# Optimization experiments

Hardware: AMD Instinct MI355X
Metric: run time of the kernel (lower is better)

The kernel has to match this reference:

```python
import jax, jax.numpy as jnp
import numpy as np
from jax.scipy.special import gammaln

# NQ_IN + 4 == 2*H is required because the two kernel=1, padding=1 convs grow the
# length axis by 4 and the following nn.Linear(2H, H) acts on the length axis.
B, NQ_IN, NK, QDIM, KDIM, H = 16, 2044, 1024, 80, 256, 1024


def setup_inputs() -> dict:
    ks = jax.random.split(jax.random.key(0), 14)
    s = 0.02
    return {
        "query": jax.random.normal(ks[0], (B, NQ_IN, QDIM), jnp.float32),
        "key": jax.random.normal(ks[1], (B, NK, KDIM), jnp.float32),
        "query_lens": jnp.full((B,), 2 * H, jnp.int32),
        "key_lens": jnp.full((B,), NK, jnp.int32),
        # query branch params (Conv1d k=1 stored as (out,in); Linear as (out,in))
        "qc1_w": jax.random.normal(ks[2], (2 * H, QDIM), jnp.float32) * s,
        "qc1_b": jax.random.normal(ks[3], (2 * H,), jnp.float32) * s,
        "qc2_w": jax.random.normal(ks[4], (2 * H, 2 * H), jnp.float32) * s,
        "qc2_b": jax.random.normal(ks[5], (2 * H,), jnp.float32) * s,
        "ql_w": jax.random.normal(ks[6], (H, 2 * H), jnp.float32) * s,
        "ql_b": jax.random.normal(ks[7], (H,), jnp.float32) * s,
        # key branch params
        "kc_w": jax.random.normal(ks[8], (H, KDIM, 3), jnp.float32) * s,
        "kc_b": jax.random.normal(ks[9], (H,), jnp.float32) * s,
        "kl1_w": jax.random.normal(ks[10], (2 * H, H), jnp.float32) * s,
        "kl1_b": jax.random.normal(ks[11], (2 * H,), jnp.float32) * s,
        "kl2_w": jax.random.normal(ks[12], (H, 2 * H), jnp.float32) * s,
        "kl2_b": jax.random.normal(ks[13], (H,), jnp.float32) * s,
    }


def _log_beta_binom(query_lens, key_lens, tq, tk):
    # Standard MAS beta-binomial alignment prior over a (tq, tk) grid.
    i = jnp.arange(tq, dtype=jnp.float32)[None, :, None]
    j = jnp.arange(tk, dtype=jnp.float32)[None, None, :]
    ql = query_lens.astype(jnp.float32)[:, None, None]
    kl = key_lens.astype(jnp.float32)[:, None, None]
    a = i + 1.0
    b = jnp.maximum(ql - i, 1.0)
    n = jnp.maximum(kl - 1.0, 0.0)
    nmj = jnp.maximum(n - j, 0.0)

    def betaln(x, y):
        return gammaln(x) + gammaln(y) - gammaln(x + y)

    logp = (gammaln(n + 1.0) - gammaln(j + 1.0) - gammaln(nmj + 1.0)
            + betaln(j + a, nmj + b) - betaln(a, b))
    valid = (i < ql) & (j < kl)
    return jnp.where(valid, logp, -1e9)


def _forward(query, key, query_lens, key_lens,
             qc1_w, qc1_b, qc2_w, qc2_b, ql_w, ql_b,
             kc_w, kc_b, kl1_w, kl1_b, kl2_w, kl2_b):
    # query branch: b n c -> b c n, two k=1/p=1 convs (pad length, pointwise), Linear over LENGTH axis
    q = jnp.transpose(query, (0, 2, 1))                       # (B, QDIM, NQ_IN)
    q = jnp.pad(q, ((0, 0), (0, 0), (1, 1)))
    q = jnp.einsum('bcn,oc->bon', q, qc1_w) + qc1_b[None, :, None]   # (B, 2H, NQ_IN+2)
    q = jnp.pad(q, ((0, 0), (0, 0), (1, 1)))
    q = jnp.einsum('bcn,oc->bon', q, qc2_w) + qc2_b[None, :, None]   # (B, 2H, 2H)
    q = jnp.einsum('bcn,hn->bch', q, ql_w) + ql_b                    # (B, 2H, H) Linear on length axis

    # key branch: b n c -> b c n, Conv1d k=3 p=1, then two Linears over LENGTH axis
    k = jnp.transpose(key, (0, 2, 1))                         # (B, KDIM, NK)
    k = jax.lax.conv_general_dilated(k, kc_w, (1,), ((1, 1),),
                                     dimension_numbers=('NCH', 'OIH', 'NCH'))
    k = k + kc_b[None, :, None]                               # (B, H, NK=H)
    k = jnp.einsum('bcn,on->bco', k, kl1_w) + kl1_b           # (B, H, 2H)
    k = jnp.einsum('bco,ho->bch', k, kl2_w) + kl2_b           # (B, H, H)

    # dist = -cdist(q, k), computed via the GEMM form (same as torch.cdist mm mode)
    sq = (jnp.sum(q * q, -1)[:, :, None] + jnp.sum(k * k, -1)[:, None, :]
          - 2.0 * jnp.einsum('bnd,bmd->bnm', q, k))           # (B, 2H, H)
    dist = -jnp.sqrt(jnp.maximum(sq, 1e-12))

    prior = _log_beta_binom(query_lens, key_lens, q.shape[1], k.shape[1])
    return jax.nn.log_softmax(dist + prior, axis=-1)


def reference(query, key, query_lens, key_lens,
              qc1_w, qc1_b, qc2_w, qc2_b, ql_w, ql_b,
              kc_w, kc_b, kl1_w, kl1_b, kl2_w, kl2_b):
    return _forward(query, key, query_lens, key_lens,
                    qc1_w, qc1_b, qc2_w, qc2_b, ql_w, ql_b,
                    kc_w, kc_b, kl1_w, kl1_b, kl2_w, kl2_b)
```

## Files before the change

### kernel.cpp

```cpp
#include <hip/hip_runtime.h>
#include <math.h>

typedef unsigned short u16;
typedef float floatx4 __attribute__((ext_vector_type(4)));
typedef __bf16 bf16x8 __attribute__((ext_vector_type(8)));

#define BB   16
#define TQ   2048
#define TK   1024
#define HH   1024
#define H2   2048
#define QD   80
#define QDP  128
#define KD   256
#define NQ   2044
#define NKEY 1024
#define T12N 3072

__device__ __forceinline__ u16 f2bf(float f) {
  unsigned int u = __float_as_uint(f);
  u = u + 0x7fffu + ((u >> 16) & 1u);
  return (u16)(u >> 16);
}
__device__ __forceinline__ float bf2f(u16 s) {
  return __uint_as_float(((unsigned int)s) << 16);
}
__device__ __forceinline__ float tgf(const float* __restrict__ tbl, int x) {
  return tbl[(x < 8191) ? (x < 0 ? 0 : x) : 8191];
}

__global__ __launch_bounds__(256) void prep_all_k(
    const float* __restrict__ qc2_w, const float* __restrict__ kl2_w,
    const float* __restrict__ ql_w, const float* __restrict__ kc_w,
    const float* __restrict__ kl1_w,
    u16* __restrict__ qc2w, u16* __restrict__ kl2w, u16* __restrict__ qlw2,
    u16* __restrict__ kcp, float* __restrict__ colsum1, float* __restrict__ tbl)
{
  long b = blockIdx.x;
  const int t = threadIdx.x;
  __shared__ float red[256];
  if (b < 16384) {
    long i = b * 256 + t; qc2w[i] = f2bf(qc2_w[i]); return;
  }
  b -= 16384;
  if (b < 8192) {
    long i = b * 256 + t; kl2w[i] = f2bf(kl2_w[i]); return;
  }
  b -= 8192;
  if (b < 8192) {
    long i = b * 256 + t;
    int n = (int)(i & 2047);
    int h = (int)(i >> 11);
    qlw2[i] = (n < NQ) ? f2bf(ql_w[(long)h * H2 + n + 2]) : (u16)0; return;
  }
  b -= 8192;
  if (b < 3072) {
    long i = b * 256 + t;
    int r = (int)(i % 768);
    int o = (int)(i / 768);
    int tt = r >> 8, d = r & 255;
    kcp[i] = f2bf(kc_w[((long)o * KD + d) * 3 + tt]); return;
  }
  b -= 3072;
  if (b < 2048) {
    const float* row = kl1_w + b * (long)HH;
    float s = row[t] + row[t + 256] + row[t + 512] + row[t + 768];
    red[t] = s; __syncthreads();
    for (int st = 128; st > 0; st >>= 1) { if (t < st) red[t] += red[t + st]; __syncthreads(); }
    if (!t) colsum1[b] = red[0];
    return;
  }
  b -= 2048;
  { int i = (int)(b * 256 + t); if (i < 8192) tbl[i] = i ? (float)lgamma((double)i) : 0.0f; }
}

__global__ __launch_bounds__(256) void tpack_k(
    const float* __restrict__ kl1_w, const float* __restrict__ qc1_w,
    const float* __restrict__ query,
    u16* __restrict__ kl1T, u16* __restrict__ qc1T, u16* __restrict__ qT)
{
  __shared__ float tile[64][65];
  int bid = blockIdx.x;
  const int tid = threadIdx.x;
  const int r4 = tid >> 6, c = tid & 63;
  const float* src; u16* dst;
  int sr0, sc0, srcR, srcC, srcStride, dstC;
  if (bid < 512) {
    sr0 = (bid >> 4) * 64; sc0 = (bid & 15) * 64;
    src = kl1_w; srcR = 2048; srcC = 1024; srcStride = 1024;
    dst = kl1T; dstC = 2048;
  } else if ((bid -= 512) < 64) {
    sr0 = (bid >> 1) * 64; sc0 = (bid & 1) * 64;
    src = qc1_w; srcR = 2048; srcC = QD; srcStride = QD;
    dst = qc1T; dstC = 2048;
  } else {
    bid -= 64;
    const int b16 = bid >> 6, r = bid & 63;
    sr0 = (r >> 1) * 64; sc0 = (r & 1) * 64;
    src = query + (long)b16 * NQ * QD; srcR = NQ; srcC = QD; srcStride = QD;
    dst = qT + (long)b16 * QDP * 2048; dstC = 2048;
  }
#pragma unroll
  for (int rr = r4; rr < 64; rr += 4) {
    const int gr = sr0 + rr, gc = sc0 + c;
    tile[rr][c] = (gr < srcR && gc < srcC) ? src[(long)gr * srcStride + gc] : 0.f;
  }
  __syncthreads();
#pragma unroll
  for (int rr = r4; rr < 64; rr += 4)
    dst[(long)(sc0 + rr) * dstC + sr0 + c] = f2bf(tile[c][rr]);
}

__global__ __launch_bounds__(256) void pack_kcolT_k(const float* __restrict__ key, u16* __restrict__ out) {
  __shared__ float tile[64][65];
  const int bid = blockIdx.x, tid = threadIdx.x;
  const int b = bid >> 6, r = bid & 63;
  const int m0 = (r >> 2) * 64;
  const int d0 = (r & 3) * 64;
  const int r4 = tid >> 6, c = tid & 63;
#pragma unroll
  for (int rr = r4; rr < 64; rr += 4)
    tile[rr][c] = key[((long)b * NKEY + m0 + rr) * KD + d0 + c];
  __syncthreads();
#pragma unroll
  for (int t = 0; t < 3; t++) {
    const int n = m0 + 1 - t + c;
    if (n >= 0 && n < NKEY) {
#pragma unroll
      for (int rr = r4; rr < 64; rr += 4)
        out[((long)b * 768 + t * 256 + d0 + rr) * NKEY + n] = f2bf(tile[c][rr]);
    }
  }
  if (m0 == 0 && c == 0) {
#pragma unroll
    for (int rr = r4; rr < 64; rr += 4)
      out[((long)b * 768 + d0 + rr) * NKEY + 0] = (u16)0;
  }
  if (m0 == 960 && c == 0) {
#pragma unroll
    for (int rr = r4; rr < 64; rr += 4)
      out[((long)b * 768 + 512 + d0 + rr) * NKEY + (NKEY - 1)] = (u16)0;
  }
}

__global__ __launch_bounds__(256) void fold_bias_k(
    const float* __restrict__ qc2_w, const float* __restrict__ qc1_b, const float* __restrict__ qc2_b,
    const float* __restrict__ kl2_w, const float* __restrict__ kl1_b, const float* __restrict__ kl2_b,
    const float* __restrict__ ql_w, const float* __restrict__ colsum1,
    float* __restrict__ bqm, float* __restrict__ bkv, float* __restrict__ s1v, float* __restrict__ s0v,
    float* __restrict__ wsum)
{
  const int bid = blockIdx.x, t = threadIdx.x;
  float s = 0.f, s2 = 0.f;
  if (bid < H2) {
    const float* row = qc2_w + (long)bid * H2;
    for (int k = t; k < H2; k += 256) s += row[k] * qc1_b[k];
  } else if (bid < H2 + HH) {
    const float* row = kl2_w + (long)(bid - H2) * H2;
    for (int k = t; k < H2; k += 256) { const float rv = row[k]; s += rv * kl1_b[k]; s2 += rv * colsum1[k]; }
  } else {
    const float* row = ql_w + (long)(bid - H2 - HH) * H2;
    for (int m = 1 + t; m <= H2 - 2; m += 256) s += row[m];
  }
  __shared__ float red[256];
  __shared__ float red2[256];
  red[t] = s; red2[t] = s2; __syncthreads();
  for (int st = 128; st > 0; st >>= 1) {
    if (t < st) { red[t] += red[t + st]; red2[t] += red2[t + st]; }
    __syncthreads();
  }
  if (!t) {
    if (bid < H2) bqm[bid] = red[0] + qc2_b[bid];
    else if (bid < H2 + HH) { bkv[bid - H2] = red[0] + kl2_b[bid - H2]; wsum[bid - H2] = red2[0]; }
    else {
      int h = bid - H2 - HH;
      s1v[h] = red[0];
      s0v[h] = ql_w[(long)h * H2] + ql_w[(long)h * H2 + H2 - 1];
    }
  }
}

__device__ __forceinline__ void gld_lds16(const u16* g, u16* l) {
  __builtin_amdgcn_global_load_lds((const __attribute__((address_space(1))) void*)g,
                                   (__attribute__((address_space(3))) void*)l, 16, 0, 0);
}

template<int OUTF32>
__global__ __launch_bounds__(256) void gemm_bt(
    const u16* __restrict__ A, const u16* __restrict__ B, void* __restrict__ Cv,
    int M, int N, int K, int lda, int ldb, int swap, int kspl,
    long sA, long sB, long sC, long sN,
    const float* __restrict__ colb, const float* __restrict__ rowb,
    const float* __restrict__ r1m, const float* __restrict__ r1n,
    const float* __restrict__ r2m, const float* __restrict__ r2n)
{
  __shared__ __align__(16) u16 As[128 * 32];
  __shared__ __align__(16) u16 Bs[128 * 32];
  const int bz = blockIdx.z;
  const int bb_ = (kspl > 1) ? bz / kspl : bz;
  const int ks_ = (kspl > 1) ? bz - bb_ * kspl : 0;
  const int tid  = threadIdx.x;
  const int lane = tid & 63;
  const int wv = tid >> 6;
  const int wm = ((tid >> 7) & 1) * 64;
  const int wn = ((tid >> 6) & 1) * 64;
  const int m0 = (swap ? blockIdx.x : blockIdx.y) * 128;
  const int n0 = (swap ? blockIdx.y : blockIdx.x) * 128;

  const int srow = wv * 32 + (lane >> 2);
  const int scol = (lane & 3) << 3;
  const u16* ga = A + bb_ * sA + (long)ks_ * K + (long)(m0 + srow) * lda + scol;
  const u16* gb = B + bb_ * sB + (long)ks_ * K + (long)(n0 + srow) * ldb + scol;
  u16* la0 = &As[(wv * 32) * 32];
  u16* la1 = &As[(wv * 32 + 16) * 32];
  u16* lb0 = &Bs[(wv * 32) * 32];
  u16* lb1 = &Bs[(wv * 32 + 16) * 32];
  const long a16 = (long)16 * lda;
  const long b16 = (long)16 * ldb;

  floatx4 acc[4][4];
#pragma unroll
  for (int a_ = 0; a_ < 4; a_++)
#pragma unroll
    for (int b_ = 0; b_ < 4; b_++) acc[a_][b_] = (floatx4){0.f, 0.f, 0.f, 0.f};

  const int fr = lane & 15;
  const int fk = (lane >> 4) << 3;

  for (int kb = 0; kb < K; kb += 32) {
    gld_lds16(ga,       la0);
    gld_lds16(ga + a16, la1);
    gld_lds16(gb,       lb0);
    gld_lds16(gb + b16, lb1);
    ga += 32; gb += 32;
    __syncthreads();
    bf16x8 af[4], bfr[4];
#pragma unroll
    for (int mi = 0; mi < 4; mi++)
      af[mi] = *reinterpret_cast<const bf16x8*>(&As[(wm + mi * 16 + fr) * 32 + fk]);
#pragma unroll
    for (int ni = 0; ni < 4; ni++)
      bfr[ni] = *reinterpret_cast<const bf16x8*>(&Bs[(wn + ni * 16 + fr) * 32 + fk]);
#pragma unroll
    for (int mi = 0; mi < 4; mi++)
#pragma unroll
      for (int ni = 0; ni < 4; ni++)
        acc[mi][ni] = __builtin_amdgcn_mfma_f32_16x16x32_bf16(af[mi], bfr[ni], acc[mi][ni], 0, 0, 0);
    __syncthreads();
  }

  const int fr4 = (lane >> 4) << 2;
  const int fc  = lane & 15;
  u16*   Cb16 = (u16*)Cv + (long)bz * sC;
  float* Cb32 = (float*)Cv + (long)bz * sC;
  const float* cbp  = colb ? colb + (long)bb_ * sN : nullptr;
  const float* r1np = r1n ? r1n + (long)bb_ * sN : nullptr;
  const float* r2np = r2n ? r2n + (long)bb_ * sN : nullptr;
#pragma unroll
  for (int mi = 0; mi < 4; mi++) {
#pragma unroll
    for (int ni = 0; ni < 4; ni++) {
      const int gm0 = m0 + wm + mi * 16 + fr4;
      const int gn  = n0 + wn + ni * 16 + fc;
      const float cbv  = cbp ? cbp[gn] : 0.f;
      const float r1nv = r1np ? r1np[gn] : 0.f;
      const float r2nv = r2np ? r2np[gn] : 0.f;
#pragma unroll
      for (int rr = 0; rr < 4; rr++) {
        const int gm = gm0 + rr;
        float v = acc[mi][ni][rr] + cbv;
        if (rowb) v += rowb[gm];
        if (r1m)  v += r1m[gm] * r1nv;
        if (r2m)  v += r2m[gm] * r2nv;
        if (OUTF32) Cb32[(long)gm * N + gn] = v;
        else        Cb16[(long)gm * N + gn] = f2bf(v);
      }
    }
  }
}

__global__ __launch_bounds__(256) void reduce_bk_k(const float* __restrict__ P, u16* __restrict__ out,
                                                   long chunk, int S, long total) {
  long j = ((long)blockIdx.x * 256 + threadIdx.x) * 4;
  if (j >= total) return;
  long b = j / chunk;
  const float* p = P + j + b * chunk * (S - 1);
  float4 s = *reinterpret_cast<const float4*>(p);
  for (int t = 1; t < S; t++) {
    const float4 v = *reinterpret_cast<const float4*>(p + (long)t * chunk);
    s.x += v.x; s.y += v.y; s.z += v.z; s.w += v.w;
  }
  union { u16 h[4]; uint2 u; } o;
  o.h[0] = f2bf(s.x); o.h[1] = f2bf(s.y); o.h[2] = f2bf(s.z); o.h[3] = f2bf(s.w);
  *reinterpret_cast<uint2*>(out + j) = o.u;
}

__global__ __launch_bounds__(256) void u_k(
    const u16* __restrict__ TpT, const float* __restrict__ qlb,
    const float* __restrict__ s1, const float* __restrict__ s0,
    const float* __restrict__ tbl, const int* __restrict__ qlens, const int* __restrict__ klens,
    float* __restrict__ u0, float* __restrict__ u1, float* __restrict__ u2,
    float* __restrict__ sc, float* __restrict__ c1,
    float* __restrict__ crow, float* __restrict__ t12)
{
  const int bid = blockIdx.x, t = threadIdx.x;
  __shared__ float4 red[256];
  if (bid < BB * QDP) {
    uint2 v = reinterpret_cast<const uint2*>(TpT + (long)bid * HH)[t];
    float a0 = bf2f((u16)(v.x & 0xffff)), a1 = bf2f((u16)(v.x >> 16));
    float a2 = bf2f((u16)(v.y & 0xffff)), a3 = bf2f((u16)(v.y >> 16));
    float4 q  = reinterpret_cast<const float4*>(qlb)[t];
    float4 w1 = reinterpret_cast<const float4*>(s1)[t];
    float4 w0 = reinterpret_cast<const float4*>(s0)[t];
    float4 s;
    s.x = a0 * q.x  + a1 * q.y  + a2 * q.z  + a3 * q.w;
    s.y = a0 * w1.x + a1 * w1.y + a2 * w1.z + a3 * w1.w;
    s.z = a0 * w0.x + a1 * w0.y + a2 * w0.z + a3 * w0.w;
    s.w = 0.f;
    red[t] = s; __syncthreads();
    for (int st = 128; st > 0; st >>= 1) {
      if (t < st) { red[t].x += red[t + st].x; red[t].y += red[t + st].y; red[t].z += red[t + st].z; }
      __syncthreads();
    }
    if (!t) { u0[bid] = red[0].x; u1[bid] = red[0].y; u2[bid] = red[0].z; }
  } else if (bid < BB * QDP + 6) {
    const int idx = bid - BB * QDP;
    const float* X = (idx == 1 || idx == 5) ? s1 : (idx == 2) ? s0 : qlb;
    const float* Y = (idx == 1 || idx == 3) ? s1 : (idx == 0) ? qlb : s0;
    float4 x = reinterpret_cast<const float4*>(X)[t];
    float4 y = reinterpret_cast<const float4*>(Y)[t];
    float4 s; s.x = x.x * y.x + x.y * y.y + x.z * y.z + x.w * y.w; s.y = s.z = s.w = 0.f;
    red[t] = s; __syncthreads();
    for (int st = 128; st > 0; st >>= 1) {
      if (t < st) red[t].x += red[t + st].x;
      __syncthreads();
    }
    if (!t) sc[idx] = red[0].x;
  } else if (bid < BB * QDP + 6 + 64) {
    const int idx = bid - (BB * QDP + 6);
    const int b = idx >> 2;
    const int j = ((idx & 3) << 8) | t;
    const int kl = klens[b];
    const int n_ = (kl - 1 > 0) ? kl - 1 : 0;
    c1[b * TK + j] = tgf(tbl, j + 1) + tgf(tbl, n_ - j + 1);
  } else if (bid < BB * QDP + 6 + 64 + 128) {
    const int idx = bid - (BB * QDP + 6 + 64);
    const int b = idx >> 3;
    const int i = ((idx & 7) << 8) | t;
    const int ql = qlens[b], kl = klens[b];
    const int n_ = (kl - 1 > 0) ? kl - 1 : 0;
    const int bb = (ql - i > 1) ? ql - i : 1;
    crow[b * TQ + i] = tgf(tbl, n_ + 1) + tgf(tbl, i + 1 + bb) - tgf(tbl, i + 1)
                     - tgf(tbl, bb) - tgf(tbl, i + 1 + n_ + bb);
  } else {
    const int idx = bid - (BB * QDP + 6 + 64 + 128);
    const int b = idx / 12;
    const int s = (idx - b * 12) * 256 + t;
    const int ql = qlens[b], kl = klens[b];
    const int n_ = (kl - 1 > 0) ? kl - 1 : 0;
    t12[b * T12N + s] = tgf(tbl, s + 1) + tgf(tbl, n_ + ql - s);
  }
}

__global__ __launch_bounds__(256) void qn_k(
    const u16* __restrict__ Wq, const float* __restrict__ WqG,
    const float* __restrict__ u0, const float* __restrict__ u1, const float* __restrict__ u2,
    const float* __restrict__ bqm, const float* __restrict__ qc2_b,
    const float* __restrict__ sc, float* __restrict__ qn)
{
  const int bx = blockIdx.x, t = threadIdx.x;
  const int b = bx >> 10;
  const int i = ((bx & 1023) << 1) | (t >> 7);
  const int d = t & 127;
  const float w  = bf2f(Wq[(long)i * QDP + d]);
  const float g  = WqG[((long)b * H2 + i) * QDP + d];
  const float bq = bqm[i], q2 = qc2_b[i];
  const float uu = u0[b * QDP + d] + bq * u1[b * QDP + d] + q2 * u2[b * QDP + d];
  __shared__ float red[256];
  red[t] = w * (g + 2.f * uu); __syncthreads();
  for (int s = 64; s > 0; s >>= 1) { if ((t & 127) < s) red[t] += red[t + s]; __syncthreads(); }
  if (d == 0) {
    const float cst = sc[0] + bq * bq * sc[1] + q2 * q2 * sc[2]
                    + 2.f * (bq * sc[3] + q2 * sc[4] + bq * q2 * sc[5]);
    qn[b * TQ + i] = red[t] + cst;
  }
}

__global__ __launch_bounds__(256) void rownormk_k(
    const u16* __restrict__ K3, const float* __restrict__ qlb,
    const float* __restrict__ s1, const float* __restrict__ s0,
    float* __restrict__ kn, float* __restrict__ yb, float* __restrict__ y1, float* __restrict__ y0)
{
  const long r = blockIdx.x;
  const int t = threadIdx.x;
  uint2 v = reinterpret_cast<const uint2*>(K3 + r * HH)[t];
  float a0 = bf2f((u16)(v.x & 0xffff)), a1 = bf2f((u16)(v.x >> 16));
  float a2 = bf2f((u16)(v.y & 0xffff)), a3 = bf2f((u16)(v.y >> 16));
  float4 q  = reinterpret_cast<const float4*>(qlb)[t];
  float4 w1 = reinterpret_cast<const float4*>(s1)[t];
  float4 w0 = reinterpret_cast<const float4*>(s0)[t];
  float4 s;
  s.x = a0 * a0   + a1 * a1   + a2 * a2   + a3 * a3;
  s.y = a0 * q.x  + a1 * q.y  + a2 * q.z  + a3 * q.w;
  s.z = a0 * w1.x + a1 * w1.y + a2 * w1.z + a3 * w1.w;
  s.w = a0 * w0.x + a1 * w0.y + a2 * w0.z + a3 * w0.w;
  __shared__ float4 red[256];
  red[t] = s; __syncthreads();
  for (int st = 128; st > 0; st >>= 1) {
    if (t < st) {
      red[t].x += red[t + st].x; red[t].y += red[t + st].y;
      red[t].z += red[t + st].z; red[t].w += red[t + st].w;
    }
    __syncthreads();
  }
  if (!t) { kn[r] = red[0].x; yb[r] = red[0].y; y1[r] = red[0].z; y0[r] = red[0].w; }
}

#define L2E 1.4426950408889634f
__global__ __launch_bounds__(512) void smax_k(
    const u16* __restrict__ Wq, const u16* __restrict__ Z2, float* __restrict__ out,
    const float* __restrict__ ybv, const float* __restrict__ y1v, const float* __restrict__ y0v,
    const float* __restrict__ bqmv, const float* __restrict__ qc2_b,
    const float* __restrict__ qnv, const float* __restrict__ knv, const float* __restrict__ c1v,
    const float* __restrict__ crowv, const float* __restrict__ t12v,
    const int* __restrict__ qlens, const int* __restrict__ klens)
{
  __shared__ float vst[64][132];
  __shared__ float t12s[1088];
  __shared__ float qns[64], crs[64], bqms[64], q2bs[64];
  __shared__ float2 lseb[4][64];
  __shared__ float lsef[64];

  const int mt = blockIdx.x, b = blockIdx.y;
  const int m0 = mt * 64;
  const int t = threadIdx.x;
  const int w = t >> 6, lane = t & 63;
  const int wm2 = (w >> 2) * 32;
  const int wn2 = (w & 3) * 32;
  const int fr = lane & 15, fk = (lane >> 4) << 3;
  const int fr4 = (lane >> 4) << 2, fc = lane & 15;
  const int qlv = qlens[b], klv = klens[b];

  if (t < 64) {
    qns[t]  = qnv[(long)b * TQ + m0 + t];
    crs[t]  = crowv[(long)b * TQ + m0 + t];
    bqms[t] = bqmv[m0 + t];
    q2bs[t] = qc2_b[m0 + t];
  }
  for (int k = t; k < 1088; k += 512) t12s[k] = t12v[(long)b * T12N + m0 + k];

  bf16x8 af[4][2];
#pragma unroll
  for (int kc = 0; kc < 4; kc++)
#pragma unroll
    for (int mi = 0; mi < 2; mi++)
      af[kc][mi] = *reinterpret_cast<const bf16x8*>(
          Wq + (long)(m0 + wm2 + mi * 16 + fr) * QDP + kc * 32 + fk);

  const u16* Zb = Z2 + (long)b * TK * QDP;
  const float* ybp = ybv + (long)b * TK;
  const float* y1p = y1v + (long)b * TK;
  const float* y0p = y0v + (long)b * TK;
  const float* knp = knv + (long)b * TK;
  const float* c1p = c1v + (long)b * TK;
  float* outp = out + (long)b * TQ * TK + (long)m0 * TK;

  float m_[8], s_[8];
#pragma unroll
  for (int ri = 0; ri < 8; ri++) { m_[ri] = -3.0e38f; s_[ri] = 0.f; }

  __syncthreads();

  for (int pass = 0; pass < 2; pass++) {
    for (int nt = 0; nt < 8; nt++) {
      bf16x8 bfr[4][2];
#pragma unroll
      for (int kc = 0; kc < 4; kc++)
#pragma unroll
        for (int nj = 0; nj < 2; nj++)
          bfr[kc][nj] = *reinterpret_cast<const bf16x8*>(
              Zb + (long)(nt * 128 + wn2 + nj * 16 + fr) * QDP + kc * 32 + fk);

      floatx4 acc[2][2];
#pragma unroll
      for (int mi = 0; mi < 2; mi++)
#pragma unroll
        for (int nj = 0; nj < 2; nj++) acc[mi][nj] = (floatx4){0.f, 0.f, 0.f, 0.f};
#pragma unroll
      for (int kc = 0; kc < 4; kc++)
#pragma unroll
        for (int mi = 0; mi < 2; mi++)
#pragma unroll
          for (int nj = 0; nj < 2; nj++)
            acc[mi][nj] = __builtin_amdgcn_mfma_f32_16x16x32_bf16(af[kc][mi], bfr[kc][nj], acc[mi][nj], 0, 0, 0);

      int gj[2]; float ybj[2], y1j[2], y0j[2], knj[2], c1j[2];
#pragma unroll
      for (int nj = 0; nj < 2; nj++) {
        gj[nj]  = nt * 128 + wn2 + nj * 16 + fc;
        ybj[nj] = ybp[gj[nj]]; y1j[nj] = y1p[gj[nj]]; y0j[nj] = y0p[gj[nj]];
        knj[nj] = knp[gj[nj]]; c1j[nj] = c1p[gj[nj]];
      }

#pragma unroll
      for (int mi = 0; mi < 2; mi++) {
#pragma unroll
        for (int rr = 0; rr < 4; rr++) {
          const int rl = wm2 + mi * 16 + fr4 + rr;
          const float qnr = qns[rl], crr = crs[rl], bqr = bqms[rl], q2r = q2bs[rl];
          float vv[2];
#pragma unroll
          for (int nj = 0; nj < 2; nj++) {
            const float Sv = acc[mi][nj][rr] + ybj[nj] + bqr * y1j[nj] + q2r * y0j[nj];
            const float sq = fmaxf(qnr + knj[nj] - 2.0f * Sv, 1e-12f);
            const float x = -__builtin_amdgcn_sqrtf(sq) + crr - c1j[nj] + t12s[rl + gj[nj]];
            vv[nj] = ((m0 + rl) < qlv && gj[nj] < klv) ? x : -1e9f;
          }
          const int ri = mi * 4 + rr;
          if (pass == 0) {
            const float nm = fmaxf(m_[ri], fmaxf(vv[0], vv[1]));
            s_[ri] = s_[ri] * exp2f((m_[ri] - nm) * L2E)
                   + exp2f((vv[0] - nm) * L2E) + exp2f((vv[1] - nm) * L2E);
            m_[ri] = nm;
          } else {
            const float l = lsef[rl];
            acc[mi][0][rr] = vv[0] - l;
            acc[mi][1][rr] = vv[1] - l;
          }
        }
      }

      if (pass == 1) {
#pragma unroll
        for (int mi = 0; mi < 2; mi++)
#pragma unroll
          for (int nj = 0; nj < 2; nj++)
#pragma unroll
            for (int rr = 0; rr < 4; rr++)
              vst[wm2 + mi * 16 + fr4 + rr][wn2 + nj * 16 + fc] = acc[mi][nj][rr];
        __syncthreads();
#pragma unroll
        for (int k = 0; k < 4; k++) {
          const int fi = k * 512 + t;
          const int row = fi >> 5, lc4 = (fi & 31) << 2;
          *reinterpret_cast<float4*>(outp + (long)row * TK + nt * 128 + lc4) =
              *reinterpret_cast<const float4*>(&vst[row][lc4]);
        }
        __syncthreads();
      }
    }

    if (pass == 0) {
#pragma unroll
      for (int k2 = 1; k2 <= 8; k2 <<= 1) {
#pragma unroll
        for (int ri = 0; ri < 8; ri++) {
          const float om = __shfl_xor(m_[ri], k2, 64);
          const float os = __shfl_xor(s_[ri], k2, 64);
          const float nm = fmaxf(m_[ri], om);
          s_[ri] = s_[ri] * exp2f((m_[ri] - nm) * L2E) + os * exp2f((om - nm) * L2E);
          m_[ri] = nm;
        }
      }
      if (fc == 0) {
#pragma unroll
        for (int mi = 0; mi < 2; mi++)
#pragma unroll
          for (int rr = 0; rr < 4; rr++)
            lseb[w & 3][wm2 + mi * 16 + fr4 + rr] = make_float2(m_[mi * 4 + rr], s_[mi * 4 + rr]);
      }
      __syncthreads();
      if (t < 64) {
        const float2 e0 = lseb[0][t], e1 = lseb[1][t], e2 = lseb[2][t], e3 = lseb[3][t];
        const float mm = fmaxf(fmaxf(e0.x, e1.x), fmaxf(e2.x, e3.x));
        const float ss = e0.y * exp2f((e0.x - mm) * L2E) + e1.y * exp2f((e1.x - mm) * L2E)
                       + e2.y * exp2f((e2.x - mm) * L2E) + e3.y * exp2f((e3.x - mm) * L2E);
        lsef[t] = mm + logf(ss);
      }
      __syncthreads();
    }
  }
}

extern "C" void kernel_launch(void* const* d_in, const int* in_sizes, int n_in,
                              void* d_out, int out_size, void* d_ws, size_t ws_size,
                              hipStream_t stream)
{
  (void)in_sizes; (void)n_in; (void)out_size; (void)ws_size;
  const float* query = (const float*)d_in[0];
  const float* key   = (const float*)d_in[1];
  const int*   qlens = (const int*)d_in[2];
  const int*   klens = (const int*)d_in[3];
  const float* qc1_w = (const float*)d_in[4];
  const float* qc1_b = (const float*)d_in[5];
  const float* qc2_w = (const float*)d_in[6];
  const float* qc2_b = (const float*)d_in[7];
  const float* ql_w  = (const float*)d_in[8];
  const float* ql_b  = (const float*)d_in[9];
  const float* kc_w  = (const float*)d_in[10];
  const float* kc_b  = (const float*)d_in[11];
  const float* kl1_w = (const float*)d_in[12];
  const float* kl1_b = (const float*)d_in[13];
  const float* kl2_w = (const float*)d_in[14];
  const float* kl2_b = (const float*)d_in[15];

  size_t off = 0;
  char* ws = (char*)d_ws;
  auto alloc = [&](size_t bytes) -> char* {
    char* p = ws + off; off += (bytes + 255) & ~(size_t)255; return p;
  };
  u16* qc2w_bf = (u16*)alloc(2ull * H2 * H2);
  u16* qc1T_bf = (u16*)alloc(2ull * QDP * H2);
  u16* kl2w_bf = (u16*)alloc(2ull * HH * H2);
  u16* kl1T_bf = (u16*)alloc(2ull * HH * H2);
  u16* qT_bf   = (u16*)alloc(2ull * BB * QDP * 2048);
  u16* kcolT_bf= (u16*)d_ws;
  u16* Z2_bf   = (u16*)d_ws;
  u16* qlw2_bf = (u16*)alloc(2ull * HH * 2048);
  u16* kcp_bf  = (u16*)alloc(2ull * HH * 768);
  u16* TpT_bf  = (u16*)alloc(2ull * H2 * HH);
  char* pool   = alloc(2ull * BB * HH * NKEY);
  float* Pbuf  = (float*)pool;
  u16* X_bf    = (u16*)pool;
  float* tbl  = (float*)alloc(4ull * 8192);
  u16* Wq_bf  = (u16*)alloc(2ull * H2 * QDP);
  u16* Wk_bf  = (u16*)alloc(2ull * HH * NKEY);
  float* bqm  = (float*)alloc(4ull * H2);
  float* bkv  = (float*)alloc(4ull * HH);
  float* s1v  = (float*)alloc(4ull * HH);
  float* s0v  = (float*)alloc(4ull * HH);
  float* wsum = (float*)alloc(4ull * HH);
  float* colsum1 = (float*)alloc(4ull * H2);
  u16* K3_bf  = (u16*)alloc(2ull * BB * TK * HH);
  float* qnv  = (float*)alloc(4ull * BB * TQ);
  float* knv  = (float*)alloc(4ull * BB * TK);
  float* ybv  = (float*)alloc(4ull * BB * TK);
  float* y1v  = (float*)alloc(4ull * BB * TK);
  float* y0v  = (float*)alloc(4ull * BB * TK);
  float* u0v  = (float*)alloc(4ull * BB * QDP);
  float* u1v  = (float*)alloc(4ull * BB * QDP);
  float* u2v  = (float*)alloc(4ull * BB * QDP);
  float* c1v  = (float*)alloc(4ull * BB * TK);
  float* crowv= (float*)alloc(4ull * BB * TQ);
  float* t12v = (float*)alloc(4ull * BB * T12N);
  float* scv  = (float*)alloc(256);
  float* WqG  = (float*)d_out;
  u16* G_bf   = (u16*)((char*)d_out + 16777216);

  prep_all_k<<<37920, 256, 0, stream>>>(qc2_w, kl2_w, ql_w, kc_w, kl1_w,
                                        qc2w_bf, kl2w_bf, qlw2_bf, kcp_bf, colsum1, tbl);
  tpack_k<<<1600, 256, 0, stream>>>(kl1_w, qc1_w, query, kl1T_bf, qc1T_bf, qT_bf);
  fold_bias_k<<<4096, 256, 0, stream>>>(qc2_w, qc1_b, qc2_b, kl2_w, kl1_b, kl2_b, ql_w, colsum1,
                                        bqm, bkv, s1v, s0v, wsum);

  gemm_bt<1><<<dim3(1, 16, 16), 256, 0, stream>>>(qc2w_bf, qc1T_bf, Pbuf, H2, QDP, 128,
      H2, H2, 0, 16, 0, 0, (long)H2 * QDP, 0,
      nullptr, nullptr, nullptr, nullptr, nullptr, nullptr);
  reduce_bk_k<<<256, 256, 0, stream>>>(Pbuf, Wq_bf, (long)H2 * QDP, 16, (long)H2 * QDP);

  gemm_bt<1><<<dim3(8, 8, 8), 256, 0, stream>>>(kl2w_bf, kl1T_bf, Pbuf, HH, NKEY, 256,
      H2, H2, 0, 8, 0, 0, (long)HH * NKEY, 0,
      nullptr, nullptr, nullptr, nullptr, nullptr, nullptr);
  reduce_bk_k<<<1024, 256, 0, stream>>>(Pbuf, Wk_bf, (long)HH * NKEY, 8, (long)HH * NKEY);

  gemm_bt<1><<<dim3(8, 16, 4), 256, 0, stream>>>(qT_bf, qlw2_bf, Pbuf, H2, HH, 512,
      2048, 2048, 0, 4, 0, 0, (long)H2 * HH, 0,
      nullptr, nullptr, nullptr, nullptr, nullptr, nullptr);
  reduce_bk_k<<<2048, 256, 0, stream>>>(Pbuf, TpT_bf, (long)H2 * HH, 4, (long)H2 * HH);

  gemm_bt<1><<<dim3(1, 1, 128), 256, 0, stream>>>(TpT_bf, TpT_bf, Pbuf, 128, 128, 128,
      HH, HH, 0, 8, (long)QDP * HH, (long)QDP * HH, 128 * 128, 0,
      nullptr, nullptr, nullptr, nullptr, nullptr, nullptr);
  reduce_bk_k<<<256, 256, 0, stream>>>(Pbuf, G_bf, 128 * 128, 8, (long)BB * 128 * 128);

  gemm_bt<1><<<dim3(1, 16, 16), 256, 0, stream>>>(Wq_bf, G_bf, WqG, H2, QDP, QDP,
      QDP, QDP, 0, 1, 0, (long)QDP * QDP, (long)H2 * QDP, 0,
      nullptr, nullptr, nullptr, nullptr, nullptr, nullptr);
  u_k<<<BB * QDP + 6 + 64 + 128 + 192, 256, 0, stream>>>(TpT_bf, ql_b, s1v, s0v, tbl, qlens, klens,
                                                         u0v, u1v, u2v, scv, c1v, crowv, t12v);
  qn_k<<<BB * TQ / 2, 256, 0, stream>>>(Wq_bf, WqG, u0v, u1v, u2v, bqm, qc2_b, scv, qnv);

  pack_kcolT_k<<<1024, 256, 0, stream>>>(key, kcolT_bf);
  gemm_bt<0><<<dim3(6, 8, BB), 256, 0, stream>>>(Wk_bf, kcolT_bf, X_bf, HH, 768, NKEY,
      NKEY, NKEY, 0, 1, 0, (long)768 * NKEY, (long)HH * 768, 0,
      nullptr, nullptr, nullptr, nullptr, nullptr, nullptr);
  gemm_bt<0><<<dim3(8, 8, BB), 256, 0, stream>>>(kcp_bf, X_bf, K3_bf, HH, NKEY, 768,
      768, 768, 1, 1, 0, (long)HH * 768, (long)TK * HH, 0,
      bkv, nullptr, kc_b, wsum, nullptr, nullptr);

  gemm_bt<1><<<dim3(8, 1, 32), 256, 0, stream>>>(K3_bf, TpT_bf, Pbuf, TK, QDP, 512,
      HH, HH, 1, 2, (long)TK * HH, (long)QDP * HH, (long)TK * QDP, 0,
      nullptr, nullptr, nullptr, nullptr, nullptr, nullptr);
  reduce_bk_k<<<2048, 256, 0, stream>>>(Pbuf, Z2_bf, (long)TK * QDP, 2, (long)BB * TK * QDP);

  rownormk_k<<<BB * TK, 256, 0, stream>>>(K3_bf, ql_b, s1v, s0v, knv, ybv, y1v, y0v);

  smax_k<<<dim3(32, 16), 512, 0, stream>>>(Wq_bf, Z2_bf, (float*)d_out,
      ybv, y1v, y0v, bqm, qc2_b, qnv, knv, c1v, crowv, t12v, qlens, klens);
}
```

Baseline: 634.4 us.

## Enlarge softmax tile to 128 rows, stage column terms in LDS, store directly

The fused distance/log-softmax kernel now runs 1024 threads per block, each block covering 128 query rows instead of 64, so the grid halves to 256 blocks. Per-column terms (key norm, bias projections, c1) are folded and preloaded into shared memory once per block, replacing repeated global loads in both passes. The LDS-staged float4 output write with its two barriers per tile is replaced by direct scalar stores from the MFMA accumulator layout. Risks: only 256 blocks for the whole GPU, and the scalar stores are less coalesced than the previous float4 stores.

```diff
diff --git a/kernel.cpp b/kernel.cpp
--- a/kernel.cpp
+++ b/kernel.cpp
@@ -417,7 +417,7 @@
 }
 
 #define L2E 1.4426950408889634f
-__global__ __launch_bounds__(512) void smax_k(
+__global__ __launch_bounds__(1024) void smax_k(
     const u16* __restrict__ Wq, const u16* __restrict__ Z2, float* __restrict__ out,
     const float* __restrict__ ybv, const float* __restrict__ y1v, const float* __restrict__ y0v,
     const float* __restrict__ bqmv, const float* __restrict__ qc2_b,
@@ -425,14 +425,14 @@
     const float* __restrict__ crowv, const float* __restrict__ t12v,
     const int* __restrict__ qlens, const int* __restrict__ klens)
 {
-  __shared__ float vst[64][132];
-  __shared__ float t12s[1088];
-  __shared__ float qns[64], crs[64], bqms[64], q2bs[64];
-  __shared__ float2 lseb[4][64];
-  __shared__ float lsef[64];
+  __shared__ float t12s[1152];
+  __shared__ float jA[1024], jB[1024], jC[1024], jc1[1024];
+  __shared__ float qns[128], crs[128], bqms[128], q2bs[128];
+  __shared__ float2 lseb[4][128];
+  __shared__ float lsef[128];
 
   const int mt = blockIdx.x, b = blockIdx.y;
-  const int m0 = mt * 64;
+  const int m0 = mt * 128;
   const int t = threadIdx.x;
   const int w = t >> 6, lane = t & 63;
   const int wm2 = (w >> 2) * 32;
@@ -441,13 +441,24 @@
   const int fr4 = (lane >> 4) << 2, fc = lane & 15;
   const int qlv = qlens[b], klv = klens[b];
 
-  if (t < 64) {
+  if (t < 128) {
     qns[t]  = qnv[(long)b * TQ + m0 + t];
     crs[t]  = crowv[(long)b * TQ + m0 + t];
     bqms[t] = bqmv[m0 + t];
     q2bs[t] = qc2_b[m0 + t];
   }
-  for (int k = t; k < 1088; k += 512) t12s[k] = t12v[(long)b * T12N + m0 + k];
+  for (int k = t; k < 1152; k += 1024) t12s[k] = t12v[(long)b * T12N + m0 + k];
+  {
+    const int j = t;
+    const float kn = knv[(long)b * TK + j];
+    const float yb = ybv[(long)b * TK + j];
+    const float y1 = y1v[(long)b * TK + j];
+    const float y0 = y0v[(long)b * TK + j];
+    jA[j]  = kn - 2.f * yb;
+    jB[j]  = -2.f * y1;
+    jC[j]  = -2.f * y0;
+    jc1[j] = c1v[(long)b * TK + j];
+  }
 
   bf16x8 af[4][2];
 #pragma unroll
@@ -458,11 +469,6 @@
           Wq + (long)(m0 + wm2 + mi * 16 + fr) * QDP + kc * 32 + fk);
 
   const u16* Zb = Z2 + (long)b * TK * QDP;
-  const float* ybp = ybv + (long)b * TK;
-  const float* y1p = y1v + (long)b * TK;
-  const float* y0p = y0v + (long)b * TK;
-  const float* knp = knv + (long)b * TK;
-  const float* c1p = c1v + (long)b * TK;
   float* outp = out + (long)b * TQ * TK + (long)m0 * TK;
 
   float m_[8], s_[8];
@@ -471,113 +477,138 @@
 
   __syncthreads();
 
-  for (int pass = 0; pass < 2; pass++) {
-    for (int nt = 0; nt < 8; nt++) {
-      bf16x8 bfr[4][2];
-#pragma unroll
-      for (int kc = 0; kc < 4; kc++)
+  for (int nt = 0; nt < 8; nt++) {
+    bf16x8 bfr[4][2];
+#pragma unroll
+    for (int kc = 0; kc < 4; kc++)
+#pragma unroll
+      for (int nj = 0; nj < 2; nj++)
+        bfr[kc][nj] = *reinterpret_cast<const bf16x8*>(
+            Zb + (long)(nt * 128 + wn2 + nj * 16 + fr) * QDP + kc * 32 + fk);
+
+    floatx4 acc[2][2];
+#pragma unroll
+    for (int mi = 0; mi < 2; mi++)
+#pragma unroll
+      for (int nj = 0; nj < 2; nj++) acc[mi][nj] = (floatx4){0.f, 0.f, 0.f, 0.f};
+#pragma unroll
+    for (int kc = 0; kc < 4; kc++)
+#pragma unroll
+      for (int mi = 0; mi < 2; mi++)
 #pragma unroll
         for (int nj = 0; nj < 2; nj++)
-          bfr[kc][nj] = *reinterpret_cast<const bf16x8*>(
-              Zb + (long)(nt * 128 + wn2 + nj * 16 + fr) * QDP + kc * 32 + fk);
-
-      floatx4 acc[2][2];
+          acc[mi][nj] = __builtin_amdgcn_mfma_f32_16x16x32_bf16(af[kc][mi], bfr[kc][nj], acc[mi][nj], 0, 0, 0);
+
+    int gj[2]; float Aj[2], Bj[2], Cj[2], Dj[2];
+#pragma unroll
+    for (int nj = 0; nj < 2; nj++) {
+      gj[nj] = nt * 128 + wn2 + nj * 16 + fc;
+      Aj[nj] = jA[gj[nj]]; Bj[nj] = jB[gj[nj]]; Cj[nj] = jC[gj[nj]]; Dj[nj] = jc1[gj[nj]];
+    }
+
+#pragma unroll
+    for (int mi = 0; mi < 2; mi++) {
+#pragma unroll
+      for (int rr = 0; rr < 4; rr++) {
+        const int rl = wm2 + mi * 16 + fr4 + rr;
+        const float qnr = qns[rl], crr = crs[rl], bqr = bqms[rl], q2r = q2bs[rl];
+        float vv[2];
+#pragma unroll
+        for (int nj = 0; nj < 2; nj++) {
+          const float sq = fmaxf(qnr + Aj[nj] + bqr * Bj[nj] + q2r * Cj[nj]
+                                 - 2.0f * acc[mi][nj][rr], 1e-12f);
+          const float x = -__builtin_amdgcn_sqrtf(sq) + crr - Dj[nj] + t12s[rl + gj[nj]];
+          vv[nj] = ((m0 + rl) < qlv && gj[nj] < klv) ? x : -1e9f;
+        }
+        const int ri = mi * 4 + rr;
+        const float nm = fmaxf(m_[ri], fmaxf(vv[0], vv[1]));
+        s_[ri] = s_[ri] * exp2f((m_[ri] - nm) * L2E)
+               + exp2f((vv[0] - nm) * L2E) + exp2f((vv[1] - nm) * L2E);
+        m_[ri] = nm;
+      }
+    }
+  }
+
+#pragma unroll
+  for (int k2 = 1; k2 <= 8; k2 <<= 1) {
+#pragma unroll
+    for (int ri = 0; ri < 8; ri++) {
+      const float om = __shfl_xor(m_[ri], k2, 64);
+      const float os = __shfl_xor(s_[ri], k2, 64);
+      const float nm = fmaxf(m_[ri], om);
+      s_[ri] = s_[ri] * exp2f((m_[ri] - nm) * L2E) + os * exp2f((om - nm) * L2E);
+      m_[ri] = nm;
+    }
+  }
+  if (fc == 0) {
+#pragma unroll
+    for (int mi = 0; mi < 2; mi++)
+#pragma unroll
+      for (int rr = 0; rr < 4; rr++)
+        lseb[w & 3][wm2 + mi * 16 + fr4 + rr] = make_float2(m_[mi * 4 + rr], s_[mi * 4 + rr]);
+  }
+  __syncthreads();
+  if (t < 128) {
+    const float2 e0 = lseb[0][t], e1 = lseb[1][t], e2 = lseb[2][t], e3 = lseb[3][t];
+    const float mm = fmaxf(fmaxf(e0.x, e1.x), fmaxf(e2.x, e3.x));
+    const float ss = e0.y * exp2f((e0.x - mm) * L2E) + e1.y * exp2f((e1.x - mm) * L2E)
+                   + e2.y * exp2f((e2.x - mm) * L2E) + e3.y * exp2f((e3.x - mm) * L2E);
+    lsef[t] = mm + logf(ss);
+  }
+  __syncthreads();
+
+  float lse_r[8];
+#pragma unroll
+  for (int mi = 0; mi < 2; mi++)
+#pragma unroll
+    for (int rr = 0; rr < 4; rr++)
+      lse_r[mi * 4 + rr] = lsef[wm2 + mi * 16 + fr4 + rr];
+
+  for (int nt = 0; nt < 8; nt++) {
+    bf16x8 bfr[4][2];
+#pragma unroll
+    for (int kc = 0; kc < 4; kc++)
+#pragma unroll
+      for (int nj = 0; nj < 2; nj++)
+        bfr[kc][nj] = *reinterpret_cast<const bf16x8*>(
+            Zb + (long)(nt * 128 + wn2 + nj * 16 + fr) * QDP + kc * 32 + fk);
+
+    floatx4 acc[2][2];
+#pragma unroll
+    for (int mi = 0; mi < 2; mi++)
+#pragma unroll
+      for (int nj = 0; nj < 2; nj++) acc[mi][nj] = (floatx4){0.f, 0.f, 0.f, 0.f};
+#pragma unroll
+    for (int kc = 0; kc < 4; kc++)
 #pragma unroll
       for (int mi = 0; mi < 2; mi++)
 #pragma unroll
-        for (int nj = 0; nj < 2; nj++) acc[mi][nj] = (floatx4){0.f, 0.f, 0.f, 0.f};
-#pragma unroll
-      for (int kc = 0; kc < 4; kc++)
-#pragma unroll
-        for (int mi = 0; mi < 2; mi++)
-#pragma unroll
-          for (int nj = 0; nj < 2; nj++)
-            acc[mi][nj] = __builtin_amdgcn_mfma_f32_16x16x32_bf16(af[kc][mi], bfr[kc][nj], acc[mi][nj], 0, 0, 0);
-
-      int gj[2]; float ybj[2], y1j[2], y0j[2], knj[2], c1j[2];
-#pragma unroll
-      for (int nj = 0; nj < 2; nj++) {
-        gj[nj]  = nt * 128 + wn2 + nj * 16 + fc;
-        ybj[nj] = ybp[gj[nj]]; y1j[nj] = y1p[gj[nj]]; y0j[nj] = y0p[gj[nj]];
-        knj[nj] = knp[gj[nj]]; c1j[nj] = c1p[gj[nj]];
-      }
-
-#pragma unroll
-      for (int mi = 0; mi < 2; mi++) {
-#pragma unroll
-        for (int rr = 0; rr < 4; rr++) {
-          const int rl = wm2 + mi * 16 + fr4 + rr;
-          const float qnr = qns[rl], crr = crs[rl], bqr = bqms[rl], q2r = q2bs[rl];
-          float vv[2];
-#pragma unroll
-          for (int nj = 0; nj < 2; nj++) {
-            const float Sv = acc[mi][nj][rr] + ybj[nj] + bqr * y1j[nj] + q2r * y0j[nj];
-            const float sq = fmaxf(qnr + knj[nj] - 2.0f * Sv, 1e-12f);
-            const float x = -__builtin_amdgcn_sqrtf(sq) + crr - c1j[nj] + t12s[rl + gj[nj]];
-            vv[nj] = ((m0 + rl) < qlv && gj[nj] < klv) ? x : -1e9f;
-          }
-          const int ri = mi * 4 + rr;
-          if (pass == 0) {
-            const float nm = fmaxf(m_[ri], fmaxf(vv[0], vv[1]));
-            s_[ri] = s_[ri] * exp2f((m_[ri] - nm) * L2E)
-                   + exp2f((vv[0] - nm) * L2E) + exp2f((vv[1] - nm) * L2E);
-            m_[ri] = nm;
-          } else {
-            const float l = lsef[rl];
-            acc[mi][0][rr] = vv[0] - l;
-            acc[mi][1][rr] = vv[1] - l;
-          }
+        for (int nj = 0; nj < 2; nj++)
+          acc[mi][nj] = __builtin_amdgcn_mfma_f32_16x16x32_bf16(af[kc][mi], bfr[kc][nj], acc[mi][nj], 0, 0, 0);
+
+    int gj[2]; float Aj[2], Bj[2], Cj[2], Dj[2];
+#pragma unroll
+    for (int nj = 0; nj < 2; nj++) {
+      gj[nj] = nt * 128 + wn2 + nj * 16 + fc;
+      Aj[nj] = jA[gj[nj]]; Bj[nj] = jB[gj[nj]]; Cj[nj] = jC[gj[nj]]; Dj[nj] = jc1[gj[nj]];
+    }
+
+#pragma unroll
+    for (int mi = 0; mi < 2; mi++) {
+#pragma unroll
+      for (int rr = 0; rr < 4; rr++) {
+        const int rl = wm2 + mi * 16 + fr4 + rr;
+        const float qnr = qns[rl], crr = crs[rl], bqr = bqms[rl], q2r = q2bs[rl];
+        const float l = lse_r[mi * 4 + rr];
+#pragma unroll
+        for (int nj = 0; nj < 2; nj++) {
+          const float sq = fmaxf(qnr + Aj[nj] + bqr * Bj[nj] + q2r * Cj[nj]
+                                 - 2.0f * acc[mi][nj][rr], 1e-12f);
+          const float x = -__builtin_amdgcn_sqrtf(sq) + crr - Dj[nj] + t12s[rl + gj[nj]];
+          const float vv = ((m0 + rl) < qlv && gj[nj] < klv) ? x : -1e9f;
+          outp[(long)rl * TK + gj[nj]] = vv - l;
         }
       }
-
-      if (pass == 1) {
-#pragma unroll
-        for (int mi = 0; mi < 2; mi++)
-#pragma unroll
-          for (int nj = 0; nj < 2; nj++)
-#pragma unroll
-            for (int rr = 0; rr < 4; rr++)
-              vst[wm2 + mi * 16 + fr4 + rr][wn2 + nj * 16 + fc] = acc[mi][nj][rr];
-        __syncthreads();
-#pragma unroll
-        for (int k = 0; k < 4; k++) {
-          const int fi = k * 512 + t;
-          const int row = fi >> 5, lc4 = (fi & 31) << 2;
-          *reinterpret_cast<float4*>(outp + (long)row * TK + nt * 128 + lc4) =
-              *reinterpret_cast<const float4*>(&vst[row][lc4]);
-        }
-        __syncthreads();
-      }
-    }
-
-    if (pass == 0) {
-#pragma unroll
-      for (int k2 = 1; k2 <= 8; k2 <<= 1) {
-#pragma unroll
-        for (int ri = 0; ri < 8; ri++) {
-          const float om = __shfl_xor(m_[ri], k2, 64);
-          const float os = __shfl_xor(s_[ri], k2, 64);
-          const float nm = fmaxf(m_[ri], om);
-          s_[ri] = s_[ri] * exp2f((m_[ri] - nm) * L2E) + os * exp2f((om - nm) * L2E);
-          m_[ri] = nm;
-        }
-      }
-      if (fc == 0) {
-#pragma unroll
-        for (int mi = 0; mi < 2; mi++)
-#pragma unroll
-          for (int rr = 0; rr < 4; rr++)
-            lseb[w & 3][wm2 + mi * 16 + fr4 + rr] = make_float2(m_[mi * 4 + rr], s_[mi * 4 + rr]);
-      }
-      __syncthreads();
-      if (t < 64) {
-        const float2 e0 = lseb[0][t], e1 = lseb[1][t], e2 = lseb[2][t], e3 = lseb[3][t];
-        const float mm = fmaxf(fmaxf(e0.x, e1.x), fmaxf(e2.x, e3.x));
-        const float ss = e0.y * exp2f((e0.x - mm) * L2E) + e1.y * exp2f((e1.x - mm) * L2E)
-                       + e2.y * exp2f((e2.x - mm) * L2E) + e3.y * exp2f((e3.x - mm) * L2E);
-        lsef[t] = mm + logf(ss);
-      }
-      __syncthreads();
     }
   }
 }
@@ -695,6 +726,6 @@
 
   rownormk_k<<<BB * TK, 256, 0, stream>>>(K3_bf, ql_b, s1v, s0v, knv, ybv, y1v, y0v);
 
-  smax_k<<<dim3(32, 16), 512, 0, stream>>>(Wq_bf, Z2_bf, (float*)d_out,
+  smax_k<<<dim3(16, 16), 1024, 0, stream>>>(Wq_bf, Z2_bf, (float*)d_out,
       ybv, y1v, y0v, bqm, qc2_b, qnv, knv, c1v, crowv, t12v, qlens, klens);
 }
```

New measurement: 616.9 us. 2.8% less time.
